# Kernel tuning notes

Hardware: AMD Instinct MI355X
Metric: run time of the kernel (lower is better)

## Reference

```python
import jax, jax.numpy as jnp
import numpy as np

NUM_NEURONS = 10000
D = 784
BATCH = 4096


def setup_inputs() -> dict:
    key = jax.random.key(0)
    kx, kw = jax.random.split(key)
    x = jax.random.normal(kx, (BATCH, D), dtype=jnp.float32)
    weights = jax.random.normal(kw, (NUM_NEURONS, D), dtype=jnp.float32)
    return {"x": x, "weights": weights}


def reference(x, weights):
    # SOM BMU lookup: squared distances between each input row and every
    # codebook row, argmin over the codebook, gather the winning neuron.
    # Use |a|^2 + |b|^2 - 2ab to avoid the (B, N, D) broadcast intermediate.
    x = x.reshape(-1, D)  # (B, D)
    x_sq = jnp.sum(x * x, axis=1, keepdims=True)          # (B, 1)
    w_sq = jnp.sum(weights * weights, axis=1)             # (N,)
    cross = x @ weights.T                                 # (B, N) GEMM
    distances = x_sq + w_sq[None, :] - 2.0 * cross        # (B, N)
    bmu_indices = jnp.argmin(distances, axis=1)           # (B,)
    bmu = jnp.take(weights, bmu_indices, axis=0)          # (B, D)
    return bmu
```

## Files before the change

kernel.cpp:

```cpp
#include <hip/hip_runtime.h>
#include <math.h>

#define BATCH 4096
#define D 784
#define N 10000

#define KP 800
#define BK 32
#define KT (KP / BK)
#define BM 128
#define BN 128
#define CPB 4
#define GX 20
#define NG GX
#define NPAD (GX * CPB * BN)
#define MARGIN 3.0f

typedef __attribute__((ext_vector_type(8))) short bh8;
typedef __attribute__((ext_vector_type(4))) float fx4;
typedef const __attribute__((address_space(1))) void CGV;
typedef __attribute__((address_space(3))) void LDSV;

static __device__ __forceinline__ unsigned short f2bf(float f) {
    unsigned u = __float_as_uint(f);
    unsigned r = u + 0x7fffu + ((u >> 16) & 1u);
    return (unsigned short)(r >> 16);
}

static __device__ __forceinline__ void top2_insert(float w, int j, float& v0, int& i0,
                                                   float& v1, int& i1) {
    if (w < v0 || (w == v0 && j < i0)) { v1 = v0; i1 = i0; v0 = w; i0 = j; }
    else if (w < v1 || (w == v1 && j < i1)) { v1 = w; i1 = j; }
}

__global__ __launch_bounds__(256) void convert_x_kernel(const float* __restrict__ x,
                                                        unsigned short* __restrict__ xh) {
    int row = blockIdx.x;
    const float4* xr = (const float4*)(x + (size_t)row * D);
    unsigned short* dst = xh + (size_t)row * KP;
    for (int i = threadIdx.x; i < KP / 4; i += 256) {
        int k = i * 4;
        uint2 o;
        if (k < D) {
            float4 v = xr[i];
            o.x = (unsigned)f2bf(v.x) | ((unsigned)f2bf(v.y) << 16);
            o.y = (unsigned)f2bf(v.z) | ((unsigned)f2bf(v.w) << 16);
        } else { o.x = 0u; o.y = 0u; }
        *(uint2*)(dst + k) = o;
    }
}

__global__ __launch_bounds__(256) void convert_w_kernel(const float* __restrict__ w,
                                                        unsigned short* __restrict__ wh,
                                                        float* __restrict__ wsq) {
    int row = blockIdx.x;
    unsigned short* dst = wh + (size_t)row * KP;
    float s = 0.f;
    if (row < N) {
        const float4* wr = (const float4*)(w + (size_t)row * D);
        for (int i = threadIdx.x; i < KP / 4; i += 256) {
            int k = i * 4;
            uint2 o;
            if (k < D) {
                float4 v = wr[i];
                s += v.x * v.x + v.y * v.y + v.z * v.z + v.w * v.w;
                o.x = (unsigned)f2bf(v.x) | ((unsigned)f2bf(v.y) << 16);
                o.y = (unsigned)f2bf(v.z) | ((unsigned)f2bf(v.w) << 16);
            } else { o.x = 0u; o.y = 0u; }
            *(uint2*)(dst + k) = o;
        }
    } else {
        for (int i = threadIdx.x; i < KP / 4; i += 256) {
            uint2 o; o.x = 0u; o.y = 0u;
            *(uint2*)(dst + i * 4) = o;
        }
    }
    __shared__ float sred[4];
    #pragma unroll
    for (int off = 32; off; off >>= 1) s += __shfl_down(s, off);
    if ((threadIdx.x & 63) == 0) sred[threadIdx.x >> 6] = s;
    __syncthreads();
    if (threadIdx.x == 0) {
        float t = sred[0] + sred[1] + sred[2] + sred[3];
        wsq[row] = (row < N) ? t : INFINITY;
    }
}

__global__ __launch_bounds__(256, 2) void dist_mfma_kernel(
    const unsigned short* __restrict__ xh, const unsigned short* __restrict__ wh,
    const float* __restrict__ wsq, float4* __restrict__ partial) {
    __shared__ __align__(16) unsigned short As[2][BM * BK];
    __shared__ __align__(16) unsigned short Bs[2][BN * BK];
    __shared__ float4 red[BM][2];

    const int tid = threadIdx.x;
    const int lane = tid & 63;
    const int wid = tid >> 6;
    const int waveM = (wid >> 1) * 64;
    const int waveN = (wid & 1) * 64;

    const int L = blockIdx.x + GX * blockIdx.y;
    const int G = (L & 7) * 80 + (L >> 3);
    const int bx = G >> 5;
    const int by = G & 31;
    const int rowBase = by * BM;
    const int colBase0 = bx * (CPB * BN);

    const int rr = tid >> 2;
    const int csw = (tid & 3) ^ ((rr >> 1) & 3);
    const unsigned short* aSrc0 = xh + (size_t)(rowBase + rr) * KP + csw * 8;
    const unsigned short* aSrc1 = aSrc0 + (size_t)64 * KP;

    char* ldsA0 = (char*)&As[0][0] + wid * 1024;
    char* ldsA1 = (char*)&As[1][0] + wid * 1024;
    char* ldsB0 = (char*)&Bs[0][0] + wid * 1024;
    char* ldsB1 = (char*)&Bs[1][0] + wid * 1024;

    int offA[4], offB[4];
    #pragma unroll
    for (int m = 0; m < 4; m++) {
        int r = waveM + m * 16 + (lane & 15);
        offA[m] = r * BK + (((lane >> 4) ^ ((r >> 1) & 3)) << 3);
    }
    #pragma unroll
    for (int n = 0; n < 4; n++) {
        int r = waveN + n * 16 + (lane & 15);
        offB[n] = r * BK + (((lane >> 4) ^ ((r >> 1) & 3)) << 3);
    }

    float V0[16], V1[16];
    int I0[16], I1[16];
    #pragma unroll
    for (int q = 0; q < 16; q++) {
        V0[q] = INFINITY; V1[q] = INFINITY;
        I0[q] = 0x7fffffff; I1[q] = 0x7fffffff;
    }

#define STAGE(nb, k0)                                                                  \
    do {                                                                               \
        __builtin_amdgcn_global_load_lds((CGV*)(aSrc0 + (k0)), (LDSV*)(ldsA##nb), 16, 0, 0);        \
        __builtin_amdgcn_global_load_lds((CGV*)(aSrc1 + (k0)), (LDSV*)(ldsA##nb + 4096), 16, 0, 0); \
        __builtin_amdgcn_global_load_lds((CGV*)(bSrc0 + (k0)), (LDSV*)(ldsB##nb), 16, 0, 0);        \
        __builtin_amdgcn_global_load_lds((CGV*)(bSrc1 + (k0)), (LDSV*)(ldsB##nb + 4096), 16, 0, 0); \
    } while (0)

#define COMPUTE(nb)                                                                    \
    do {                                                                               \
        bh8 af[4], bf[4];                                                              \
        _Pragma("unroll")                                                              \
        for (int m = 0; m < 4; m++) af[m] = *(const bh8*)&As[nb][offA[m]];             \
        _Pragma("unroll")                                                              \
        for (int n = 0; n < 4; n++) bf[n] = *(const bh8*)&Bs[nb][offB[n]];             \
        _Pragma("unroll")                                                              \
        for (int m = 0; m < 4; m++)                                                    \
            _Pragma("unroll")                                                          \
            for (int n = 0; n < 4; n++)                                                \
                acc[m][n] = __builtin_amdgcn_mfma_f32_16x16x32_bf16(af[m], bf[n],      \
                                                                    acc[m][n], 0, 0, 0); \
    } while (0)

#define VM0 asm volatile("s_waitcnt vmcnt(0)" ::: "memory")
#define BARR __builtin_amdgcn_s_barrier()

    #pragma unroll 1
    for (int c = 0; c < CPB; ++c) {
        const int colBase = colBase0 + c * BN;
        const unsigned short* bSrc0 = wh + (size_t)(colBase + rr) * KP + csw * 8;
        const unsigned short* bSrc1 = bSrc0 + (size_t)64 * KP;

        fx4 acc[4][4];
        #pragma unroll
        for (int m = 0; m < 4; m++)
            #pragma unroll
            for (int n = 0; n < 4; n++) acc[m][n] = (fx4)0.f;

        STAGE(0, 0);
        VM0; BARR;
        #pragma unroll 1
        for (int t = 0; t < KT - 1; t += 2) {
            STAGE(1, (t + 1) * BK);
            COMPUTE(0);
            VM0; BARR;
            STAGE(0, (t + 2) * BK);
            COMPUTE(1);
            VM0; BARR;
        }
        COMPUTE(0);

        const int cb = colBase + waveN + (lane & 15);
        #pragma unroll
        for (int n = 0; n < 4; n++) {
            const float wq = wsq[cb + n * 16];
            const int ci = cb + n * 16;
            #pragma unroll
            for (int m = 0; m < 4; m++)
                #pragma unroll
                for (int r = 0; r < 4; r++) {
                    float dv = wq - 2.f * acc[m][n][r];
                    top2_insert(dv, ci, V0[m * 4 + r], I0[m * 4 + r],
                                V1[m * 4 + r], I1[m * 4 + r]);
                }
        }
        __syncthreads();
    }

#undef STAGE
#undef COMPUTE
#undef VM0
#undef BARR

    #pragma unroll
    for (int q = 0; q < 16; q++) {
        float v0 = V0[q], v1 = V1[q];
        int i0 = I0[q], i1 = I1[q];
        #pragma unroll
        for (int mask = 1; mask < 16; mask <<= 1) {
            float w0 = __shfl_xor(v0, mask); int j0 = __shfl_xor(i0, mask);
            float w1 = __shfl_xor(v1, mask); int j1 = __shfl_xor(i1, mask);
            top2_insert(w0, j0, v0, i0, v1, i1);
            top2_insert(w1, j1, v0, i0, v1, i1);
        }
        if ((lane & 15) == 0) {
            int m = q >> 2, r = q & 3;
            int row_local = waveM + m * 16 + (lane >> 4) * 4 + r;
            red[row_local][wid & 1] =
                make_float4(v0, __int_as_float(i0), v1, __int_as_float(i1));
        }
    }
    __syncthreads();
    if (tid < BM) {
        float4 pa = red[tid][0], pb = red[tid][1];
        float v0 = pa.x, v1 = pa.z;
        int i0 = __float_as_int(pa.y), i1 = __float_as_int(pa.w);
        top2_insert(pb.x, __float_as_int(pb.y), v0, i0, v1, i1);
        top2_insert(pb.z, __float_as_int(pb.w), v0, i0, v1, i1);
        partial[(size_t)(rowBase + tid) * NG + bx] =
            make_float4(v0, __int_as_float(i0), v1, __int_as_float(i1));
    }
}

__global__ __launch_bounds__(256) void rescore_kernel(const float* __restrict__ x,
                                                      const float* __restrict__ w,
                                                      const float4* __restrict__ partial,
                                                      float* __restrict__ out) {
    int wid = threadIdx.x >> 6, lane = threadIdx.x & 63;
    int row = blockIdx.x * 4 + wid;
    __shared__ int s_cnt[4];
    __shared__ int s_cand[4][64];

    const float4* part = partial + (size_t)row * NG;

    float bv = INFINITY;
    for (int c = lane; c < NG; c += 64) bv = fminf(bv, part[c].x);
    #pragma unroll
    for (int mask = 1; mask < 64; mask <<= 1) bv = fminf(bv, __shfl_xor(bv, mask));
    float thr = bv + MARGIN;

    if (lane == 0) s_cnt[wid] = 0;
    __syncthreads();
    for (int c = lane; c < NG; c += 64) {
        float4 p = part[c];
        if (p.x <= thr) {
            int pos = atomicAdd(&s_cnt[wid], 1);
            if (pos < 64) s_cand[wid][pos] = __float_as_int(p.y);
        }
        if (p.z <= thr) {
            int pos = atomicAdd(&s_cnt[wid], 1);
            if (pos < 64) s_cand[wid][pos] = __float_as_int(p.w);
        }
    }
    __syncthreads();
    int cnt = s_cnt[wid]; if (cnt > 64) cnt = 64;

    double bd = INFINITY; int bi = 0x7fffffff;
    for (int c = 0; c < cnt; c++) {
        int idx = s_cand[wid][c];
        const float* wr = w + (size_t)idx * D;
        const float* xr = x + (size_t)row * D;
        double s = 0.0;
        for (int d = lane; d < D; d += 64) {
            double wv = (double)wr[d];
            s += wv * (wv - 2.0 * (double)xr[d]);
        }
        #pragma unroll
        for (int mask = 1; mask < 64; mask <<= 1) s += __shfl_xor(s, mask);
        if (s < bd || (s == bd && idx < bi)) { bd = s; bi = idx; }
    }

    const float4* src = (const float4*)(w + (size_t)bi * D);
    float4* dst = (float4*)(out + (size_t)row * D);
    for (int i = lane; i < D / 4; i += 64) dst[i] = src[i];
}

extern "C" void kernel_launch(void* const* d_in, const int* in_sizes, int n_in,
                              void* d_out, int out_size, void* d_ws, size_t ws_size,
                              hipStream_t stream) {
    const float* x = (const float*)d_in[0];
    const float* w = (const float*)d_in[1];
    float* out = (float*)d_out;

    const size_t off_xh = 0;
    const size_t off_wh = off_xh + (size_t)BATCH * KP * 2;
    const size_t off_wsq = off_wh + (size_t)NPAD * KP * 2;
    const size_t off_part = off_wsq + (size_t)NPAD * 4;

    unsigned short* xh = (unsigned short*)((char*)d_ws + off_xh);
    unsigned short* wh = (unsigned short*)((char*)d_ws + off_wh);
    float* wsq = (float*)((char*)d_ws + off_wsq);
    float4* partial = (float4*)((char*)d_ws + off_part);

    hipLaunchKernelGGL(convert_x_kernel, dim3(BATCH), dim3(256), 0, stream, x, xh);
    hipLaunchKernelGGL(convert_w_kernel, dim3(NPAD), dim3(256), 0, stream, w, wh, wsq);
    hipLaunchKernelGGL(dist_mfma_kernel, dim3(GX, BATCH / BM), dim3(256), 0, stream,
                       xh, wh, wsq, partial);
    hipLaunchKernelGGL(rescore_kernel, dim3(BATCH / 4), dim3(256), 0, stream,
                       x, w, partial, out);
}
```

Before: 472.7 us.

## Split distance GEMM across more column blocks with runtime grid width

Replaces the fixed 20x32 grid, where each block looped over 4 column tiles, with a runtime grid width of up to 80 and one column tile per block. It falls back to 40 or 20 when the workspace cannot hold the larger partial buffer. Launch bounds rise to 4 waves per SIMD and the block-to-XCD remap is rewritten so row tiles are grouped per XCD. The aim is more parallel blocks and better occupancy. The cost is more partial top-2 entries for the rescore pass to scan, and possible register pressure from the tighter launch bound.

```diff
diff --git a/kernel.cpp b/kernel.cpp
--- a/kernel.cpp
+++ b/kernel.cpp
@@ -10,10 +10,8 @@
 #define KT (KP / BK)
 #define BM 128
 #define BN 128
-#define CPB 4
-#define GX 20
-#define NG GX
-#define NPAD (GX * CPB * BN)
+#define GXMAX 80
+#define NPAD (GXMAX * BN)
 #define MARGIN 3.0f
 
 typedef __attribute__((ext_vector_type(8))) short bh8;
@@ -86,9 +84,10 @@
     }
 }
 
-__global__ __launch_bounds__(256, 2) void dist_mfma_kernel(
+__global__ __launch_bounds__(256, 4) void dist_mfma_kernel(
     const unsigned short* __restrict__ xh, const unsigned short* __restrict__ wh,
-    const float* __restrict__ wsq, float4* __restrict__ partial) {
+    const float* __restrict__ wsq, float4* __restrict__ partial,
+    int gx, int cpb) {
     __shared__ __align__(16) unsigned short As[2][BM * BK];
     __shared__ __align__(16) unsigned short Bs[2][BN * BK];
     __shared__ float4 red[BM][2];
@@ -99,12 +98,13 @@
     const int waveM = (wid >> 1) * 64;
     const int waveN = (wid & 1) * 64;
 
-    const int L = blockIdx.x + GX * blockIdx.y;
-    const int G = (L & 7) * 80 + (L >> 3);
-    const int bx = G >> 5;
-    const int by = G & 31;
+    const int L = blockIdx.x + gx * blockIdx.y;
+    const int xcd = L & 7;
+    const int s = L >> 3;
+    const int bx = s >> 2;
+    const int by = xcd * 4 + (s & 3);
     const int rowBase = by * BM;
-    const int colBase0 = bx * (CPB * BN);
+    const int colBase0 = bx * (cpb * BN);
 
     const int rr = tid >> 2;
     const int csw = (tid & 3) ^ ((rr >> 1) & 3);
@@ -163,7 +163,7 @@
 #define BARR __builtin_amdgcn_s_barrier()
 
     #pragma unroll 1
-    for (int c = 0; c < CPB; ++c) {
+    for (int c = 0; c < cpb; ++c) {
         const int colBase = colBase0 + c * BN;
         const unsigned short* bSrc0 = wh + (size_t)(colBase + rr) * KP + csw * 8;
         const unsigned short* bSrc1 = bSrc0 + (size_t)64 * KP;
@@ -234,7 +234,7 @@
         int i0 = __float_as_int(pa.y), i1 = __float_as_int(pa.w);
         top2_insert(pb.x, __float_as_int(pb.y), v0, i0, v1, i1);
         top2_insert(pb.z, __float_as_int(pb.w), v0, i0, v1, i1);
-        partial[(size_t)(rowBase + tid) * NG + bx] =
+        partial[(size_t)(rowBase + tid) * gx + bx] =
             make_float4(v0, __int_as_float(i0), v1, __int_as_float(i1));
     }
 }
@@ -242,23 +242,23 @@
 __global__ __launch_bounds__(256) void rescore_kernel(const float* __restrict__ x,
                                                       const float* __restrict__ w,
                                                       const float4* __restrict__ partial,
-                                                      float* __restrict__ out) {
+                                                      float* __restrict__ out, int ng) {
     int wid = threadIdx.x >> 6, lane = threadIdx.x & 63;
     int row = blockIdx.x * 4 + wid;
     __shared__ int s_cnt[4];
     __shared__ int s_cand[4][64];
 
-    const float4* part = partial + (size_t)row * NG;
+    const float4* part = partial + (size_t)row * ng;
 
     float bv = INFINITY;
-    for (int c = lane; c < NG; c += 64) bv = fminf(bv, part[c].x);
+    for (int c = lane; c < ng; c += 64) bv = fminf(bv, part[c].x);
     #pragma unroll
     for (int mask = 1; mask < 64; mask <<= 1) bv = fminf(bv, __shfl_xor(bv, mask));
     float thr = bv + MARGIN;
 
     if (lane == 0) s_cnt[wid] = 0;
     __syncthreads();
-    for (int c = lane; c < NG; c += 64) {
+    for (int c = lane; c < ng; c += 64) {
         float4 p = part[c];
         if (p.x <= thr) {
             int pos = atomicAdd(&s_cnt[wid], 1);
@@ -304,6 +304,10 @@
     const size_t off_wsq = off_wh + (size_t)NPAD * KP * 2;
     const size_t off_part = off_wsq + (size_t)NPAD * 4;
 
+    int gx = 80, cpb = 1;
+    if (ws_size < off_part + (size_t)BATCH * 80 * 16) { gx = 40; cpb = 2; }
+    if (ws_size < off_part + (size_t)BATCH * 40 * 16) { gx = 20; cpb = 4; }
+
     unsigned short* xh = (unsigned short*)((char*)d_ws + off_xh);
     unsigned short* wh = (unsigned short*)((char*)d_ws + off_wh);
     float* wsq = (float*)((char*)d_ws + off_wsq);
@@ -311,8 +315,8 @@
 
     hipLaunchKernelGGL(convert_x_kernel, dim3(BATCH), dim3(256), 0, stream, x, xh);
     hipLaunchKernelGGL(convert_w_kernel, dim3(NPAD), dim3(256), 0, stream, w, wh, wsq);
-    hipLaunchKernelGGL(dist_mfma_kernel, dim3(GX, BATCH / BM), dim3(256), 0, stream,
-                       xh, wh, wsq, partial);
+    hipLaunchKernelGGL(dist_mfma_kernel, dim3(gx, 32), dim3(256), 0, stream,
+                       xh, wh, wsq, partial, gx, cpb);
     hipLaunchKernelGGL(rescore_kernel, dim3(BATCH / 4), dim3(256), 0, stream,
-                       x, w, partial, out);
-}
+                       x, w, partial, out, gx);
+}
```

New measurement: 570.8 us. +20.7%, slower.
